# Performance work log

Measured on AMD Instinct MI355X. Metric: run time of the kernel, lower is better.

## Reference

```python
import jax, jax.numpy as jnp
import numpy as np

B, S, F = 16, 1024, 768
GRID_SIZE = 5
SPLINE_ORDER = 3
GRID_MIN, GRID_MAX = -1.5, 1.5
EPS = 1e-8  # denominator guard, as in the source


def setup_inputs() -> dict:
    key = jax.random.key(0)
    kx, kc = jax.random.split(key)
    x = jax.random.normal(kx, (B, S, F), dtype=jnp.float32)
    # learned knots: per-feature copy of linspace(grid_range, grid_size)
    knots = jnp.tile(jnp.linspace(GRID_MIN, GRID_MAX, GRID_SIZE, dtype=jnp.float32), (F, 1))  # (F, G)
    coeffs = jax.random.normal(kc, (F, GRID_SIZE + SPLINE_ORDER - 1), dtype=jnp.float32)       # (F, G+k-1)
    scaler = jnp.ones((F,), dtype=jnp.float32)
    return {"x": x, "knots": knots, "coeffs": coeffs, "scaler": scaler}


def _extend_knots(knots, order):
    # pad `order` uniformly-spaced knots on each side: (F, G) -> (F, G + 2*order)
    step = (knots[:, -1] - knots[:, 0]) / (knots.shape[1] - 1)          # (F,)
    left = knots[:, :1] - step[:, None] * jnp.arange(order, 0, -1, dtype=knots.dtype)
    right = knots[:, -1:] + step[:, None] * jnp.arange(1, order + 1, dtype=knots.dtype)
    return jnp.concatenate([left, knots, right], axis=1)


def _bspline_basis(x2d, t_ext, order):
    # x2d: (N, F); t_ext: (F, K). Cox-de Boor, vectorized over basis index.
    t = t_ext[None]          # (1, F, K)
    xe = x2d[..., None]      # (N, F, 1)
    # degree 0: indicator of knot interval -> (N, F, K-1)
    b = ((xe >= t[..., :-1]) & (xe < t[..., 1:])).astype(x2d.dtype)
    for d in range(1, order + 1):
        left = (xe - t[..., :-(d + 1)]) / (t[..., d:-1] - t[..., :-(d + 1)] + EPS) * b[..., :-1]
        right = (t[..., d + 1:] - xe) / (t[..., d + 1:] - t[..., 1:-d] + EPS) * b[..., 1:]
        b = left + right
    return b                 # (N, F, K-1-order)


def reference(x, knots, coeffs, scaler):
    Bsz, Ssz, Feat = x.shape
    x2d = x.reshape(-1, Feat)                       # (N, F)
    t = _extend_knots(knots, SPLINE_ORDER)          # (F, G + 2k)
    basis = _bspline_basis(x2d, t, SPLINE_ORDER)    # (N, F, G+k-1)
    out = jnp.einsum('nfj,fj->nf', basis, coeffs) * scaler
    return out.reshape(Bsz, Ssz, Feat)
```

## Files before the change

kernel.cpp:

```cpp
#include <hip/hip_runtime.h>


constexpr int FEAT  = 768;
constexpr int GSZ   = 5;
constexpr int NCOEF = 7;
constexpr int BLK   = 256;
constexpr int NBLK  = 1536;
constexpr int PT    = 15;

__device__ __forceinline__ float eval_one(float x, float invh, float nt0h,
                                          const float* __restrict__ clds,
                                          int base)
{
    const float g  = fmaf(x, invh, nt0h);
    const float fi = floorf(g);
    const int   i  = (int)fi;
    const float w  = g - fi;
    const float omw = 1.0f - w;
    const float w2 = w * w,     w3 = w2 * w;
    const float o2 = omw * omw, o3 = o2 * omw;
    const float W0 = o3 * (1.0f / 6.0f);
    const float W3 = w3 * (1.0f / 6.0f);
    const float W1 = fmaf(0.5f, w3, 2.0f / 3.0f) - w2;
    const float W2 = fmaf(0.5f, o3, 2.0f / 3.0f) - o2;
    const int jb = i - 3;

    float acc = 0.0f;
#pragma unroll
    for (int m = 0; m < 4; ++m) {
        const int  jj    = jb + m;
        const bool valid = (unsigned)jj <= 6u;
        const int  jc    = min(max(jj, 0), 6);
        const float c    = clds[base + jc];
        const float Wm   = (m == 0) ? W0 : (m == 1) ? W1 : (m == 2) ? W2 : W3;
        acc = fmaf(valid ? Wm : 0.0f, c, acc);
    }
    return acc;
}

__global__ __launch_bounds__(256)
void kan_uniform(const float* __restrict__ xg,
                 const float* __restrict__ knots,
                 const float* __restrict__ coeffs,
                 const float* __restrict__ scaler,
                 float* __restrict__ outg,
                 long n2)
{
    __shared__ float clds[BLK * PT];

    const int  t  = threadIdx.x;
    const long e0 = (long)blockIdx.x * BLK + t;
    const int  f0 = (int)((2 * e0) % FEAT);

    float invh[2], nt0h[2];
#pragma unroll
    for (int c = 0; c < 2; ++c) {
        const int f  = f0 + c;
        const float k0 = knots[f * GSZ];
        const float k4 = knots[f * GSZ + GSZ - 1];
        const float h  = (k4 - k0) * 0.25f;
        const float iv = 1.0f / h;
        invh[c] = iv;
        nt0h[c] = 3.0f - k0 * iv;
        const float sc = scaler[f];
#pragma unroll
        for (int j = 0; j < NCOEF; ++j)
            clds[t * PT + c * NCOEF + j] = coeffs[f * NCOEF + j] * sc;
    }
    __syncthreads();

    const float2* __restrict__ xp = (const float2*)xg;
    float2*       __restrict__ op = (float2*)outg;
    const long stride = (long)NBLK * BLK;
    const int  b0 = t * PT;
    const int  b1 = t * PT + NCOEF;

#pragma unroll 2
    for (long e = e0; e < n2; e += stride) {
        const float2 v = xp[e];
        float2 r;
        r.x = eval_one(v.x, invh[0], nt0h[0], clds, b0);
        r.y = eval_one(v.y, invh[1], nt0h[1], clds, b1);
        op[e] = r;
    }
}

extern "C" void kernel_launch(void* const* d_in, const int* in_sizes, int n_in,
                              void* d_out, int out_size, void* d_ws, size_t ws_size,
                              hipStream_t stream) {
    const float* x      = (const float*)d_in[0];
    const float* knots  = (const float*)d_in[1];
    const float* coeffs = (const float*)d_in[2];
    const float* scaler = (const float*)d_in[3];
    float* out = (float*)d_out;

    const long n2 = (long)in_sizes[0] / 2;

    kan_uniform<<<dim3(NBLK), dim3(BLK), 0, stream>>>(
        x, knots, coeffs, scaler, out, n2);
}
```

Baseline: 109.5 us.

## Pad coefficient table with zeros, transpose LDS layout, and batch four loads per iteration

Stores the per-thread coefficient table in LDS as zero-padded, column-major-by-thread rows so that the four taps use one base index plus constant offsets, with no per-tap clamping or validity selects. The strided layout also removes LDS bank conflicts from the old 15-float per-thread stride. The main loop is manually unrolled to issue four independent float2 loads before computing, adding memory-level parallelism. LDS use grows from 15 to 26 floats per thread, and the out-of-range zeroing now depends on the padded rows and a single range check.

New measurement: 110.9 us. About the same (+1.3%).

```diff
diff --git a/kernel.cpp b/kernel.cpp
--- a/kernel.cpp
+++ b/kernel.cpp
@@ -4,39 +4,9 @@
 constexpr int FEAT  = 768;
 constexpr int GSZ   = 5;
 constexpr int NCOEF = 7;
+constexpr int TPF   = 13;
 constexpr int BLK   = 256;
 constexpr int NBLK  = 1536;
-constexpr int PT    = 15;
-
-__device__ __forceinline__ float eval_one(float x, float invh, float nt0h,
-                                          const float* __restrict__ clds,
-                                          int base)
-{
-    const float g  = fmaf(x, invh, nt0h);
-    const float fi = floorf(g);
-    const int   i  = (int)fi;
-    const float w  = g - fi;
-    const float omw = 1.0f - w;
-    const float w2 = w * w,     w3 = w2 * w;
-    const float o2 = omw * omw, o3 = o2 * omw;
-    const float W0 = o3 * (1.0f / 6.0f);
-    const float W3 = w3 * (1.0f / 6.0f);
-    const float W1 = fmaf(0.5f, w3, 2.0f / 3.0f) - w2;
-    const float W2 = fmaf(0.5f, o3, 2.0f / 3.0f) - o2;
-    const int jb = i - 3;
-
-    float acc = 0.0f;
-#pragma unroll
-    for (int m = 0; m < 4; ++m) {
-        const int  jj    = jb + m;
-        const bool valid = (unsigned)jj <= 6u;
-        const int  jc    = min(max(jj, 0), 6);
-        const float c    = clds[base + jc];
-        const float Wm   = (m == 0) ? W0 : (m == 1) ? W1 : (m == 2) ? W2 : W3;
-        acc = fmaf(valid ? Wm : 0.0f, c, acc);
-    }
-    return acc;
-}
 
 __global__ __launch_bounds__(256)
 void kan_uniform(const float* __restrict__ xg,
@@ -46,7 +16,7 @@
                  float* __restrict__ outg,
                  long n2)
 {
-    __shared__ float clds[BLK * PT];
+    __shared__ float clds[2 * TPF * BLK];
 
     const int  t  = threadIdx.x;
     const long e0 = (long)blockIdx.x * BLK + t;
@@ -55,7 +25,7 @@
     float invh[2], nt0h[2];
 #pragma unroll
     for (int c = 0; c < 2; ++c) {
-        const int f  = f0 + c;
+        const int   f  = f0 + c;
         const float k0 = knots[f * GSZ];
         const float k4 = knots[f * GSZ + GSZ - 1];
         const float h  = (k4 - k0) * 0.25f;
@@ -64,23 +34,63 @@
         nt0h[c] = 3.0f - k0 * iv;
         const float sc = scaler[f];
 #pragma unroll
+        for (int j = 0; j < 3; ++j) {
+            clds[(c * TPF + j) * BLK + t]      = 0.0f;
+            clds[(c * TPF + 10 + j) * BLK + t] = 0.0f;
+        }
+#pragma unroll
         for (int j = 0; j < NCOEF; ++j)
-            clds[t * PT + c * NCOEF + j] = coeffs[f * NCOEF + j] * sc;
+            clds[(c * TPF + 3 + j) * BLK + t] = coeffs[f * NCOEF + j] * sc;
     }
     __syncthreads();
+
+    auto eval = [&](float x, int c) -> float {
+        const float g  = fmaf(x, invh[c], nt0h[c]);
+        const float fi = floorf(g);
+        const int   i  = (int)fi;
+        const float w  = g - fi;
+        const bool  inr = ((unsigned)i < 10u);
+        const int   ic  = min(max(i, 0), 9);
+        const float o  = 1.0f - w;
+        const float w2 = w * w,  w3 = w2 * w;
+        const float o2 = o * o,  o3 = o2 * o;
+        const float W0 = o3 * (1.0f / 6.0f);
+        const float W3 = w3 * (1.0f / 6.0f);
+        const float W1 = fmaf(0.5f, w3, 2.0f / 3.0f) - w2;
+        const float W2 = fmaf(0.5f, o3, 2.0f / 3.0f) - o2;
+        const float* p = &clds[(c * TPF + ic) * BLK + t];
+        float acc =      W0 * p[0];
+        acc = fmaf(W1, p[BLK],     acc);
+        acc = fmaf(W2, p[2 * BLK], acc);
+        acc = fmaf(W3, p[3 * BLK], acc);
+        return inr ? acc : 0.0f;
+    };
 
     const float2* __restrict__ xp = (const float2*)xg;
     float2*       __restrict__ op = (float2*)outg;
     const long stride = (long)NBLK * BLK;
-    const int  b0 = t * PT;
-    const int  b1 = t * PT + NCOEF;
 
-#pragma unroll 2
-    for (long e = e0; e < n2; e += stride) {
+    long e = e0;
+    for (; e + 3 * stride < n2; e += 4 * stride) {
+        const float2 v0 = xp[e];
+        const float2 v1 = xp[e + stride];
+        const float2 v2 = xp[e + 2 * stride];
+        const float2 v3 = xp[e + 3 * stride];
+        float2 r0, r1, r2, r3;
+        r0.x = eval(v0.x, 0); r0.y = eval(v0.y, 1);
+        r1.x = eval(v1.x, 0); r1.y = eval(v1.y, 1);
+        r2.x = eval(v2.x, 0); r2.y = eval(v2.y, 1);
+        r3.x = eval(v3.x, 0); r3.y = eval(v3.y, 1);
+        op[e]              = r0;
+        op[e + stride]     = r1;
+        op[e + 2 * stride] = r2;
+        op[e + 3 * stride] = r3;
+    }
+    for (; e < n2; e += stride) {
         const float2 v = xp[e];
         float2 r;
-        r.x = eval_one(v.x, invh[0], nt0h[0], clds, b0);
-        r.y = eval_one(v.y, invh[1], nt0h[1], clds, b1);
+        r.x = eval(v.x, 0);
+        r.y = eval(v.y, 1);
         op[e] = r;
     }
 }
```
